# Kernel optimization log

Hardware: AMD Instinct MI355X
Metric: run time of the kernel (lower is better)

## Reference

```python
import math
import jax, jax.numpy as jnp
import numpy as np

B = 2
IN_DIM = 512
OUT_DIM = 256
MAX_IN_SEQ = 1024
MAX_OUT_SEQ = 512
SEQ = 1024  # actual_seq_len == max_in_seq
LN_EPS = 1e-5
TWO_PI = 2.0 * math.pi


def setup_inputs() -> dict:
    key = jax.random.key(0)
    ks = jax.random.split(key, 4)
    x = jax.random.normal(ks[0], (B * SEQ, IN_DIM), dtype=jnp.float32)
    M = jax.random.uniform(ks[1], (OUT_DIM, IN_DIM), minval=-0.5, maxval=0.5, dtype=jnp.float32)
    P = jax.random.uniform(ks[2], (OUT_DIM, OUT_DIM), minval=-0.1, maxval=0.1, dtype=jnp.float32)
    Linker = jax.random.uniform(ks[3], (MAX_IN_SEQ, MAX_OUT_SEQ), minval=-0.1, maxval=0.1, dtype=jnp.float32)
    ln_gamma = jnp.ones((OUT_DIM,), dtype=jnp.float32)
    ln_beta = jnp.zeros((OUT_DIM,), dtype=jnp.float32)
    return {"x": x, "M": M, "P": P, "Linker": Linker,
            "ln_gamma": ln_gamma, "ln_beta": ln_beta, "actual_seq_len": SEQ}


def _periods(out_dim):
    # periods[i, j] = i * out_dim + j + 2
    i = jnp.arange(out_dim, dtype=jnp.float32)[:, None]
    j = jnp.arange(out_dim, dtype=jnp.float32)[None, :]
    return i * out_dim + j + 2.0


def _layernorm(z, gamma, beta):
    mu = jnp.mean(z, axis=-1, keepdims=True)
    var = jnp.mean(jnp.square(z - mu), axis=-1, keepdims=True)
    return (z - mu) * jax.lax.rsqrt(var + LN_EPS) * gamma + beta


def reference(x, M, P, Linker, ln_gamma, ln_beta, actual_seq_len):
    total, _ = x.shape                      # (B*S, in_dim)
    batch = total // actual_seq_len
    out_seq = max(1, actual_seq_len // 2)   # reduction_factor = 2

    # projection + LayerNorm
    Z = x @ M.T                             # (B*S, out_dim)
    Zn = _layernorm(Z, ln_gamma, ln_beta)

    # position-dependent cos-weighted transform over the flattened B*S axis
    periods = _periods(OUT_DIM)             # (O, O)
    k = jnp.arange(total, dtype=jnp.float32)  # (B*S,)
    phi = jnp.cos(TWO_PI * k[:, None, None] / periods[None])  # (B*S, O, O)
    T = jnp.einsum('kj,ij,kij->ki', Zn, P, phi)               # (B*S, O)

    # adaptive sequence-length reduction via Linker
    AL = Linker[:actual_seq_len, :out_seq]  # (S, S')
    T3 = T.reshape(batch, actual_seq_len, OUT_DIM)
    U = jnp.einsum('bso,st->bto', T3, AL).reshape(batch * out_seq, OUT_DIM)

    # shared residual: reuse M and Linker on the pre-LN projection
    R3 = Z.reshape(batch, actual_seq_len, OUT_DIM)
    R = jnp.einsum('bso,st->bto', R3, AL).reshape(batch * out_seq, OUT_DIM)

    return U + R, out_seq
```

## Files before the change

### kernel.cpp

```cpp
#include <hip/hip_runtime.h>
#include <hip/hip_bf16.h>

#define TOT     2048
#define INDIM   512
#define OD      256
#define SEQL    1024
#define TQ      512
#define NB      2
#define LN_EPS  1e-5f

#define JSPL    16
#define JW      (OD / JSPL)
#define K3SPL   4

typedef __attribute__((ext_vector_type(8))) short bf16x8;
typedef __attribute__((ext_vector_type(4))) float f32x4;
typedef __attribute__((ext_vector_type(2))) float f32x2;

__device__ __forceinline__ short f2bf(float f) {
    __hip_bfloat16 h = __float2bfloat16(f);
    return *(short*)&h;
}
__device__ __forceinline__ uint pack2(float a, float b) {
    return (uint)(ushort)f2bf(a) | ((uint)(ushort)f2bf(b) << 16);
}

__global__ __launch_bounds__(256) void kALt(
    const float* __restrict__ L, short* __restrict__ ALt)
{
    __shared__ float tl[32][36];
    const int tt = blockIdx.x;
    const int s0 = (tt >> 4) * 32;
    const int t0 = (tt & 15) * 32;
    const int tid = threadIdx.x;
    const int r  = tid >> 3;
    const int c4 = (tid & 7) * 4;
    float4 v = *(const float4*)(L + (size_t)(s0 + r) * TQ + t0 + c4);
    tl[r][c4 + 0] = v.x; tl[r][c4 + 1] = v.y;
    tl[r][c4 + 2] = v.z; tl[r][c4 + 3] = v.w;
    __syncthreads();
    uint lo = pack2(tl[c4 + 0][r], tl[c4 + 1][r]);
    uint hi = pack2(tl[c4 + 2][r], tl[c4 + 3][r]);
    *(uint2*)(ALt + (size_t)(t0 + r) * SEQL + s0 + c4) = make_uint2(lo, hi);
}

template<bool CVT>
__device__ __forceinline__ void mfma_tile64(
    const void* __restrict__ Av, int lda,
    const void* __restrict__ Bv, int ldb,
    float* __restrict__ C, int ldc,
    int r0, int c0, int k0, int nk)
{
    __shared__ short Al[64][40];
    __shared__ short Bl[64][40];
    const int tid = threadIdx.x;
    const int w   = tid >> 6;
    const int wm  = w >> 1, wn = w & 1;
    const int l   = tid & 63;
    const int lr  = l & 15, lg = l >> 4;
    const int srow = tid >> 2, skg = (tid & 3) * 8;

    f32x4 acc[2][2] = {{{0.f,0.f,0.f,0.f},{0.f,0.f,0.f,0.f}},
                       {{0.f,0.f,0.f,0.f},{0.f,0.f,0.f,0.f}}};

    for (int ks = 0; ks < nk; ++ks) {
        const int kb = k0 + ks * 32;
        __syncthreads();
        if (CVT) {
            const float* Af = (const float*)Av;
            const float* Bf = (const float*)Bv;
            const float* ar = Af + (size_t)(r0 + srow) * lda + kb + skg;
            float4 a0 = *(const float4*)ar, a1 = *(const float4*)(ar + 4);
            *(uint4*)&Al[srow][skg] = make_uint4(pack2(a0.x, a0.y), pack2(a0.z, a0.w),
                                                 pack2(a1.x, a1.y), pack2(a1.z, a1.w));
            const float* br = Bf + (size_t)(c0 + srow) * ldb + kb + skg;
            float4 b0 = *(const float4*)br, b1 = *(const float4*)(br + 4);
            *(uint4*)&Bl[srow][skg] = make_uint4(pack2(b0.x, b0.y), pack2(b0.z, b0.w),
                                                 pack2(b1.x, b1.y), pack2(b1.z, b1.w));
        } else {
            const short* As = (const short*)Av;
            const short* Bs = (const short*)Bv;
            *(bf16x8*)&Al[srow][skg] = *(const bf16x8*)(As + (size_t)(r0 + srow) * lda + kb + skg);
            *(bf16x8*)&Bl[srow][skg] = *(const bf16x8*)(Bs + (size_t)(c0 + srow) * ldb + kb + skg);
        }
        __syncthreads();
        bf16x8 a0 = *(const bf16x8*)&Al[wm * 32 +      lr][lg * 8];
        bf16x8 a1 = *(const bf16x8*)&Al[wm * 32 + 16 + lr][lg * 8];
        bf16x8 b0 = *(const bf16x8*)&Bl[wn * 32 +      lr][lg * 8];
        bf16x8 b1 = *(const bf16x8*)&Bl[wn * 32 + 16 + lr][lg * 8];
        acc[0][0] = __builtin_amdgcn_mfma_f32_16x16x32_bf16(a0, b0, acc[0][0], 0, 0, 0);
        acc[0][1] = __builtin_amdgcn_mfma_f32_16x16x32_bf16(a0, b1, acc[0][1], 0, 0, 0);
        acc[1][0] = __builtin_amdgcn_mfma_f32_16x16x32_bf16(a1, b0, acc[1][0], 0, 0, 0);
        acc[1][1] = __builtin_amdgcn_mfma_f32_16x16x32_bf16(a1, b1, acc[1][1], 0, 0, 0);
    }
#pragma unroll
    for (int sm = 0; sm < 2; ++sm)
#pragma unroll
    for (int sn = 0; sn < 2; ++sn)
#pragma unroll
    for (int q = 0; q < 4; ++q)
        C[(size_t)(r0 + wm * 32 + sm * 16 + 4 * lg + q) * ldc
          + (c0 + wn * 32 + sn * 16 + lr)] = acc[sm][sn][q];
}

__global__ __launch_bounds__(256, 4) void k1_mfma(
    const float* __restrict__ x, const float* __restrict__ M,
    float* __restrict__ Zp)
{
    mfma_tile64<true>(x, INDIM, M, INDIM,
                      Zp + (size_t)blockIdx.z * TOT * OD, OD,
                      blockIdx.x * 64, blockIdx.y * 64, blockIdx.z * 256, 8);
}

__global__ __launch_bounds__(256) void k1b_ln(
    const float* __restrict__ Zp,
    const float* __restrict__ gamma, const float* __restrict__ beta,
    float* __restrict__ Z, float* __restrict__ Zn)
{
    const int r0 = blockIdx.x * 8;
    const int c  = threadIdx.x;

    float acc[8];
#pragma unroll
    for (int r = 0; r < 8; ++r) {
        const size_t i = (size_t)(r0 + r) * OD + c;
        acc[r] = Zp[i] + Zp[(size_t)TOT * OD + i];
    }

    __shared__ float s1[8][4], s2[8][4];
    const int lane = c & 63;
    const int wid  = c >> 6;
#pragma unroll
    for (int r = 0; r < 8; ++r) {
        float s = acc[r], q = acc[r] * acc[r];
#pragma unroll
        for (int off = 32; off > 0; off >>= 1) {
            s += __shfl_xor(s, off, 64);
            q += __shfl_xor(q, off, 64);
        }
        if (lane == 0) { s1[r][wid] = s; s2[r][wid] = q; }
    }
    __syncthreads();
#pragma unroll
    for (int r = 0; r < 8; ++r) {
        float s  = s1[r][0] + s1[r][1] + s1[r][2] + s1[r][3];
        float q  = s2[r][0] + s2[r][1] + s2[r][2] + s2[r][3];
        float mu = s * (1.f / OD);
        float var = q * (1.f / OD) - mu * mu;
        float inv = rsqrtf(var + LN_EPS);
        float z  = acc[r];
        float zn = (z - mu) * inv * gamma[c] + beta[c];
        Z [(size_t)(r0 + r) * OD + c] = z;
        Zn[(size_t)(r0 + r) * OD + c] = zn;
    }
}

__global__ __launch_bounds__(128) void k2_t(
    const float* __restrict__ Zn, const float* __restrict__ P,
    short* __restrict__ Tp)
{
    const int k0 = blockIdx.x * 64;
    const int i0 = blockIdx.y * 128;
    const int j0 = blockIdx.z * JW;

    __shared__ float znT[JW][68];
    __shared__ float ptT[JW][132];

    const int tid = threadIdx.x;
    {
        const int row = tid & 63;
        const int jh  = (tid >> 6) * 8;
        const float* zr = Zn + (size_t)(k0 + row) * OD + j0 + jh;
        float4 v0 = *(const float4*)(zr);
        float4 v1 = *(const float4*)(zr + 4);
        znT[jh + 0][row] = v0.x; znT[jh + 1][row] = v0.y;
        znT[jh + 2][row] = v0.z; znT[jh + 3][row] = v0.w;
        znT[jh + 4][row] = v1.x; znT[jh + 5][row] = v1.y;
        znT[jh + 6][row] = v1.z; znT[jh + 7][row] = v1.w;
        const float* pr = P + (size_t)(i0 + tid) * OD + j0;
        float4 p0 = *(const float4*)(pr);
        float4 p1 = *(const float4*)(pr + 4);
        float4 p2 = *(const float4*)(pr + 8);
        float4 p3 = *(const float4*)(pr + 12);
        ptT[ 0][tid] = p0.x; ptT[ 1][tid] = p0.y; ptT[ 2][tid] = p0.z; ptT[ 3][tid] = p0.w;
        ptT[ 4][tid] = p1.x; ptT[ 5][tid] = p1.y; ptT[ 6][tid] = p1.z; ptT[ 7][tid] = p1.w;
        ptT[ 8][tid] = p2.x; ptT[ 9][tid] = p2.y; ptT[10][tid] = p2.z; ptT[11][tid] = p2.w;
        ptT[12][tid] = p3.x; ptT[13][tid] = p3.y; ptT[14][tid] = p3.z; ptT[15][tid] = p3.w;
    }
    __syncthreads();

    const int kg = tid >> 6;
    const int l  = tid & 63;
    const int il = 2 * l;
    const float kbase = (float)(k0 + kg * 32);
    const float pbA   = (float)((i0 + il) * OD + j0 + 2);

    f32x2 accA[16], accB[16];
#pragma unroll
    for (int m = 0; m < 16; ++m) { accA[m] = (f32x2){0.f, 0.f}; accB[m] = (f32x2){0.f, 0.f}; }

    const float* zrow = &znT[0][kg * 32];

    for (int j = 0; j < JW; ++j) {
        f32x2 wp = *(const f32x2*)&ptT[j][il];
        const float pA  = pbA + (float)j;
        const float ipA = __builtin_amdgcn_rcpf(pA);
        const float aA  = __builtin_amdgcn_fractf(kbase * ipA);
        const float c0A = __builtin_amdgcn_cosf(aA);
        const float s0A = __builtin_amdgcn_sinf(aA);
        const float cdA = __builtin_amdgcn_cosf(ipA);
        const float sdA = __builtin_amdgcn_sinf(ipA);
        const float c1A = c0A * cdA - s0A * sdA;
        const float s1A = s0A * cdA + c0A * sdA;
        const float c2A = c1A * cdA - s1A * sdA;
        const float c3A = c2A * cdA - (s1A * cdA + c1A * sdA) * sdA;
        const float r2A = 2.f * (1.f - 2.f * sdA * sdA);
        f32x2 DA_p = {wp.x * c0A, wp.x * c1A};
        f32x2 DA_c = {wp.x * c2A, wp.x * c3A};
        const f32x2 RA = {r2A, r2A};
        const float pB  = pA + 256.f;
        const float ipB = __builtin_amdgcn_rcpf(pB);
        const float aB  = __builtin_amdgcn_fractf(kbase * ipB);
        const float c0B = __builtin_amdgcn_cosf(aB);
        const float s0B = __builtin_amdgcn_sinf(aB);
        const float cdB = __builtin_amdgcn_cosf(ipB);
        const float sdB = __builtin_amdgcn_sinf(ipB);
        const float c1B = c0B * cdB - s0B * sdB;
        const float s1B = s0B * cdB + c0B * sdB;
        const float c2B = c1B * cdB - s1B * sdB;
        const float c3B = c2B * cdB - (s1B * cdB + c1B * sdB) * sdB;
        const float r2B = 2.f * (1.f - 2.f * sdB * sdB);
        f32x2 DB_p = {wp.y * c0B, wp.y * c1B};
        f32x2 DB_c = {wp.y * c2B, wp.y * c3B};
        const f32x2 RB = {r2B, r2B};

        const float* zc = zrow + (size_t)j * 68;
#pragma unroll
        for (int m = 0; m < 8; ++m) {
            float4 z4 = *(const float4*)(zc + 4 * m);
            f32x2 zlo = {z4.x, z4.y};
            f32x2 zhi = {z4.z, z4.w};
            accA[2 * m    ] += zlo * DA_p;
            accB[2 * m    ] += zlo * DB_p;
            f32x2 tA = RA * DA_c - DA_p;  DA_p = DA_c;  DA_c = tA;
            f32x2 tB = RB * DB_c - DB_p;  DB_p = DB_c;  DB_c = tB;
            accA[2 * m + 1] += zhi * DA_p;
            accB[2 * m + 1] += zhi * DB_p;
            tA = RA * DA_c - DA_p;  DA_p = DA_c;  DA_c = tA;
            tB = RB * DB_c - DB_p;  DB_p = DB_c;  DB_c = tB;
        }
    }

    short* Tpl = Tp + (size_t)blockIdx.z * (TOT * OD);
    const int ia = i0 + il;
    const int kb = k0 + kg * 32;
#pragma unroll
    for (int m = 0; m < 16; ++m) {
        *(uint*)(Tpl + (size_t)(kb + 2 * m    ) * OD + ia) = pack2(accA[m].x, accB[m].x);
        *(uint*)(Tpl + (size_t)(kb + 2 * m + 1) * OD + ia) = pack2(accA[m].y, accB[m].y);
    }
}

__global__ __launch_bounds__(256) void k2b_w(
    const float* __restrict__ Z, const short* __restrict__ Tp,
    short* __restrict__ Wt)
{
    __shared__ float tl[32][36];
    const int kt0 = blockIdx.x * 32;
    const int o0  = blockIdx.y * 32;
    const int tid = threadIdx.x;
    const int r   = tid >> 3;
    const int c4  = (tid & 7) * 4;

    const size_t idx = (size_t)(kt0 + r) * OD + o0 + c4;
    float4 z = *(const float4*)(Z + idx);
#pragma unroll
    for (int p = 0; p < JSPL; ++p) {
        uint2 t = *(const uint2*)(Tp + (size_t)p * (TOT * OD) + idx);
        z.x += __uint_as_float(t.x << 16);
        z.y += __uint_as_float(t.x & 0xFFFF0000u);
        z.z += __uint_as_float(t.y << 16);
        z.w += __uint_as_float(t.y & 0xFFFF0000u);
    }
    *(float4*)&tl[r][c4] = z;
    __syncthreads();

    const int ol = tid >> 3;
    const int sc = (tid & 7) * 4;
    const int b  = kt0 >> 10;
    const int sb = kt0 & 1023;
    uint lo = pack2(tl[sc + 0][ol], tl[sc + 1][ol]);
    uint hi = pack2(tl[sc + 2][ol], tl[sc + 3][ol]);
    *(uint2*)(Wt + ((size_t)b * OD + o0 + ol) * SEQL + sb + sc) = make_uint2(lo, hi);
}

__global__ __launch_bounds__(256, 4) void k3_mfma(
    const short* __restrict__ ALt, const short* __restrict__ Wt,
    float* __restrict__ Op)
{
    const int b   = blockIdx.z & 1;
    const int ksp = blockIdx.z >> 1;
    mfma_tile64<false>(ALt, SEQL, Wt + (size_t)b * OD * SEQL, SEQL,
                       Op + (size_t)ksp * (NB * TQ * OD) + (size_t)b * TQ * OD, OD,
                       blockIdx.x * 64, blockIdx.y * 64, ksp * (SEQL / K3SPL), (SEQL / K3SPL) / 32);
}

__global__ __launch_bounds__(256) void k4_comb(
    const float* __restrict__ Op, float* __restrict__ out, int out_size)
{
    const int m = blockIdx.x * 256 + threadIdx.x;
    const int N4 = (NB * TQ * OD) / 4;
    if (m < N4) {
        float4 a = ((const float4*)Op)[m];
#pragma unroll
        for (int p = 1; p < K3SPL; ++p) {
            float4 t = ((const float4*)(Op + (size_t)p * (NB * TQ * OD)))[m];
            a.x += t.x; a.y += t.y; a.z += t.z; a.w += t.w;
        }
        ((float4*)out)[m] = a;
    }
    if (m == 0 && out_size > NB * TQ * OD)
        out[NB * TQ * OD] = (float)TQ;
}

extern "C" void kernel_launch(void* const* d_in, const int* in_sizes, int n_in,
                              void* d_out, int out_size, void* d_ws, size_t ws_size,
                              hipStream_t stream)
{
    const float* x  = (const float*)d_in[0];
    const float* M  = (const float*)d_in[1];
    const float* P  = (const float*)d_in[2];
    const float* L  = (const float*)d_in[3];
    const float* g  = (const float*)d_in[4];
    const float* be = (const float*)d_in[5];
    float* out = (float*)d_out;

    float* ws_f = (float*)d_ws;
    float* Zp = ws_f;
    float* Z  = Zp + 2 * (size_t)TOT * OD;
    float* Zn = Z  + (size_t)TOT * OD;
    float* Op = Zn + (size_t)TOT * OD;
    short* ALt = (short*)(Op + (size_t)K3SPL * NB * TQ * OD);
    short* Wt  = ALt + (size_t)TQ * SEQL;
    short* Tp  = Wt  + (size_t)NB * OD * SEQL;

    kALt<<<512, 256, 0, stream>>>(L, ALt);
    k1_mfma<<<dim3(TOT / 64, OD / 64, 2), 256, 0, stream>>>(x, M, Zp);
    k1b_ln<<<TOT / 8, 256, 0, stream>>>(Zp, g, be, Z, Zn);
    k2_t<<<dim3(TOT / 64, OD / 128, JSPL), 128, 0, stream>>>(Zn, P, Tp);
    k2b_w<<<dim3(TOT / 32, OD / 32), 256, 0, stream>>>(Z, Tp, Wt);
    k3_mfma<<<dim3(TQ / 64, OD / 64, NB * K3SPL), 256, 0, stream>>>(ALt, Wt, Op);
    k4_comb<<<(NB * TQ * OD / 4 + 255) / 256, 256, 0, stream>>>(Op, out, out_size);
}
```

Before: 48.95 us.

## Fuse LN, split-K reductions and Linker transpose into producer kernels via last-block counters

Collapses seven launches into a memset plus three kernels. The LN row statistics, the Tp partial sum, and the k3 split-K combine now run in whichever block finishes last for each tile, detected with an atomic counter and threadfence. LN normalization is applied on the fly when loading into k2, and k3 reads the fp32 Linker and W directly, transposing and converting them to bf16 in LDS. This removes launch overhead and intermediate buffers (Z, Zn, ALt, Wt), at the cost of tail work serialized in the last blocks and strided, uncoalesced LDS transposes in k3.

```diff
diff --git a/kernel.cpp b/kernel.cpp
--- a/kernel.cpp
+++ b/kernel.cpp
@@ -24,25 +24,8 @@
 __device__ __forceinline__ uint pack2(float a, float b) {
     return (uint)(ushort)f2bf(a) | ((uint)(ushort)f2bf(b) << 16);
 }
-
-__global__ __launch_bounds__(256) void kALt(
-    const float* __restrict__ L, short* __restrict__ ALt)
-{
-    __shared__ float tl[32][36];
-    const int tt = blockIdx.x;
-    const int s0 = (tt >> 4) * 32;
-    const int t0 = (tt & 15) * 32;
-    const int tid = threadIdx.x;
-    const int r  = tid >> 3;
-    const int c4 = (tid & 7) * 4;
-    float4 v = *(const float4*)(L + (size_t)(s0 + r) * TQ + t0 + c4);
-    tl[r][c4 + 0] = v.x; tl[r][c4 + 1] = v.y;
-    tl[r][c4 + 2] = v.z; tl[r][c4 + 3] = v.w;
-    __syncthreads();
-    uint lo = pack2(tl[c4 + 0][r], tl[c4 + 1][r]);
-    uint hi = pack2(tl[c4 + 2][r], tl[c4 + 3][r]);
-    *(uint2*)(ALt + (size_t)(t0 + r) * SEQL + s0 + c4) = make_uint2(lo, hi);
-}
+__device__ __forceinline__ float bflo(uint t) { return __uint_as_float(t << 16); }
+__device__ __forceinline__ float bfhi(uint t) { return __uint_as_float(t & 0xFFFF0000u); }
 
 template<bool CVT>
 __device__ __forceinline__ void mfma_tile64(
@@ -105,59 +88,46 @@
 
 __global__ __launch_bounds__(256, 4) void k1_mfma(
     const float* __restrict__ x, const float* __restrict__ M,
-    float* __restrict__ Zp)
+    float* __restrict__ Zp, float* __restrict__ muv, float* __restrict__ inv,
+    int* __restrict__ cnt)
 {
     mfma_tile64<true>(x, INDIM, M, INDIM,
                       Zp + (size_t)blockIdx.z * TOT * OD, OD,
                       blockIdx.x * 64, blockIdx.y * 64, blockIdx.z * 256, 8);
-}
-
-__global__ __launch_bounds__(256) void k1b_ln(
-    const float* __restrict__ Zp,
+
+    __threadfence();
+    __syncthreads();
+    __shared__ int lastf;
+    if (threadIdx.x == 0)
+        lastf = (atomicAdd(&cnt[blockIdx.x], 1) == 7);
+    __syncthreads();
+    if (!lastf) return;
+
+    const int row  = blockIdx.x * 64 + (threadIdx.x >> 2);
+    const int part = threadIdx.x & 3;
+    const float* z0 = Zp + (size_t)row * OD + part * 64;
+    const float* z1 = z0 + (size_t)TOT * OD;
+    float s = 0.f, q = 0.f;
+#pragma unroll 8
+    for (int c = 0; c < 64; ++c) {
+        float v = z0[c] + z1[c];
+        s += v; q += v * v;
+    }
+    s += __shfl_xor(s, 1); q += __shfl_xor(q, 1);
+    s += __shfl_xor(s, 2); q += __shfl_xor(q, 2);
+    if (part == 0) {
+        float m  = s * (1.f / OD);
+        float vr = q * (1.f / OD) - m * m;
+        muv[row] = m;
+        inv[row] = rsqrtf(vr + LN_EPS);
+    }
+}
+
+__global__ __launch_bounds__(128) void k2_t(
+    const float* __restrict__ Zp, const float* __restrict__ muv, const float* __restrict__ inv,
     const float* __restrict__ gamma, const float* __restrict__ beta,
-    float* __restrict__ Z, float* __restrict__ Zn)
-{
-    const int r0 = blockIdx.x * 8;
-    const int c  = threadIdx.x;
-
-    float acc[8];
-#pragma unroll
-    for (int r = 0; r < 8; ++r) {
-        const size_t i = (size_t)(r0 + r) * OD + c;
-        acc[r] = Zp[i] + Zp[(size_t)TOT * OD + i];
-    }
-
-    __shared__ float s1[8][4], s2[8][4];
-    const int lane = c & 63;
-    const int wid  = c >> 6;
-#pragma unroll
-    for (int r = 0; r < 8; ++r) {
-        float s = acc[r], q = acc[r] * acc[r];
-#pragma unroll
-        for (int off = 32; off > 0; off >>= 1) {
-            s += __shfl_xor(s, off, 64);
-            q += __shfl_xor(q, off, 64);
-        }
-        if (lane == 0) { s1[r][wid] = s; s2[r][wid] = q; }
-    }
-    __syncthreads();
-#pragma unroll
-    for (int r = 0; r < 8; ++r) {
-        float s  = s1[r][0] + s1[r][1] + s1[r][2] + s1[r][3];
-        float q  = s2[r][0] + s2[r][1] + s2[r][2] + s2[r][3];
-        float mu = s * (1.f / OD);
-        float var = q * (1.f / OD) - mu * mu;
-        float inv = rsqrtf(var + LN_EPS);
-        float z  = acc[r];
-        float zn = (z - mu) * inv * gamma[c] + beta[c];
-        Z [(size_t)(r0 + r) * OD + c] = z;
-        Zn[(size_t)(r0 + r) * OD + c] = zn;
-    }
-}
-
-__global__ __launch_bounds__(128) void k2_t(
-    const float* __restrict__ Zn, const float* __restrict__ P,
-    short* __restrict__ Tp)
+    const float* __restrict__ P, short* __restrict__ Tp,
+    float* __restrict__ W, int* __restrict__ cnt)
 {
     const int k0 = blockIdx.x * 64;
     const int i0 = blockIdx.y * 128;
@@ -170,13 +140,25 @@
     {
         const int row = tid & 63;
         const int jh  = (tid >> 6) * 8;
-        const float* zr = Zn + (size_t)(k0 + row) * OD + j0 + jh;
-        float4 v0 = *(const float4*)(zr);
-        float4 v1 = *(const float4*)(zr + 4);
-        znT[jh + 0][row] = v0.x; znT[jh + 1][row] = v0.y;
-        znT[jh + 2][row] = v0.z; znT[jh + 3][row] = v0.w;
-        znT[jh + 4][row] = v1.x; znT[jh + 5][row] = v1.y;
-        znT[jh + 6][row] = v1.z; znT[jh + 7][row] = v1.w;
+        const size_t base = (size_t)(k0 + row) * OD + j0 + jh;
+        float4 a0 = *(const float4*)(Zp + base);
+        float4 a1 = *(const float4*)(Zp + base + 4);
+        float4 b0 = *(const float4*)(Zp + (size_t)TOT * OD + base);
+        float4 b1 = *(const float4*)(Zp + (size_t)TOT * OD + base + 4);
+        const float m  = muv[k0 + row];
+        const float iv = inv[k0 + row];
+        float4 g0 = *(const float4*)(gamma + j0 + jh);
+        float4 g1 = *(const float4*)(gamma + j0 + jh + 4);
+        float4 e0 = *(const float4*)(beta + j0 + jh);
+        float4 e1 = *(const float4*)(beta + j0 + jh + 4);
+        znT[jh + 0][row] = (a0.x + b0.x - m) * iv * g0.x + e0.x;
+        znT[jh + 1][row] = (a0.y + b0.y - m) * iv * g0.y + e0.y;
+        znT[jh + 2][row] = (a0.z + b0.z - m) * iv * g0.z + e0.z;
+        znT[jh + 3][row] = (a0.w + b0.w - m) * iv * g0.w + e0.w;
+        znT[jh + 4][row] = (a1.x + b1.x - m) * iv * g1.x + e1.x;
+        znT[jh + 5][row] = (a1.y + b1.y - m) * iv * g1.y + e1.y;
+        znT[jh + 6][row] = (a1.z + b1.z - m) * iv * g1.z + e1.z;
+        znT[jh + 7][row] = (a1.w + b1.w - m) * iv * g1.w + e1.w;
         const float* pr = P + (size_t)(i0 + tid) * OD + j0;
         float4 p0 = *(const float4*)(pr);
         float4 p1 = *(const float4*)(pr + 4);
@@ -259,67 +241,120 @@
         *(uint*)(Tpl + (size_t)(kb + 2 * m    ) * OD + ia) = pack2(accA[m].x, accB[m].x);
         *(uint*)(Tpl + (size_t)(kb + 2 * m + 1) * OD + ia) = pack2(accA[m].y, accB[m].y);
     }
-}
-
-__global__ __launch_bounds__(256) void k2b_w(
-    const float* __restrict__ Z, const short* __restrict__ Tp,
-    short* __restrict__ Wt)
-{
-    __shared__ float tl[32][36];
-    const int kt0 = blockIdx.x * 32;
-    const int o0  = blockIdx.y * 32;
-    const int tid = threadIdx.x;
-    const int r   = tid >> 3;
-    const int c4  = (tid & 7) * 4;
-
-    const size_t idx = (size_t)(kt0 + r) * OD + o0 + c4;
-    float4 z = *(const float4*)(Z + idx);
-#pragma unroll
-    for (int p = 0; p < JSPL; ++p) {
-        uint2 t = *(const uint2*)(Tp + (size_t)p * (TOT * OD) + idx);
-        z.x += __uint_as_float(t.x << 16);
-        z.y += __uint_as_float(t.x & 0xFFFF0000u);
-        z.z += __uint_as_float(t.y << 16);
-        z.w += __uint_as_float(t.y & 0xFFFF0000u);
-    }
-    *(float4*)&tl[r][c4] = z;
-    __syncthreads();
-
-    const int ol = tid >> 3;
-    const int sc = (tid & 7) * 4;
-    const int b  = kt0 >> 10;
-    const int sb = kt0 & 1023;
-    uint lo = pack2(tl[sc + 0][ol], tl[sc + 1][ol]);
-    uint hi = pack2(tl[sc + 2][ol], tl[sc + 3][ol]);
-    *(uint2*)(Wt + ((size_t)b * OD + o0 + ol) * SEQL + sb + sc) = make_uint2(lo, hi);
+
+    __threadfence();
+    __syncthreads();
+    __shared__ int lastf;
+    if (tid == 0)
+        lastf = (atomicAdd(&cnt[blockIdx.x * 2 + blockIdx.y], 1) == JSPL - 1);
+    __syncthreads();
+    if (!lastf) return;
+
+#pragma unroll
+    for (int e = 0; e < 32; ++e) {
+        const int lin = e * 128 + tid;
+        const int r   = lin >> 6;
+        const int c2  = (lin & 63) * 2;
+        const size_t addr = (size_t)(k0 + r) * OD + i0 + c2;
+        float wx = Zp[addr]     + Zp[(size_t)TOT * OD + addr];
+        float wy = Zp[addr + 1] + Zp[(size_t)TOT * OD + addr + 1];
+#pragma unroll
+        for (int p = 0; p < JSPL; ++p) {
+            uint t = *(const uint*)(Tp + (size_t)p * (TOT * OD) + addr);
+            wx += bflo(t); wy += bfhi(t);
+        }
+        *(f32x2*)(W + addr) = (f32x2){wx, wy};
+    }
 }
 
 __global__ __launch_bounds__(256, 4) void k3_mfma(
-    const short* __restrict__ ALt, const short* __restrict__ Wt,
-    float* __restrict__ Op)
+    const float* __restrict__ L, const float* __restrict__ W,
+    float* __restrict__ Op, float* __restrict__ out, int out_size,
+    int* __restrict__ cnt)
 {
     const int b   = blockIdx.z & 1;
     const int ksp = blockIdx.z >> 1;
-    mfma_tile64<false>(ALt, SEQL, Wt + (size_t)b * OD * SEQL, SEQL,
-                       Op + (size_t)ksp * (NB * TQ * OD) + (size_t)b * TQ * OD, OD,
-                       blockIdx.x * 64, blockIdx.y * 64, ksp * (SEQL / K3SPL), (SEQL / K3SPL) / 32);
-}
-
-__global__ __launch_bounds__(256) void k4_comb(
-    const float* __restrict__ Op, float* __restrict__ out, int out_size)
-{
-    const int m = blockIdx.x * 256 + threadIdx.x;
-    const int N4 = (NB * TQ * OD) / 4;
-    if (m < N4) {
-        float4 a = ((const float4*)Op)[m];
+    const int r0  = blockIdx.x * 64;
+    const int c0  = blockIdx.y * 64;
+    const int k0  = ksp * (SEQL / K3SPL);
+
+    __shared__ short Al[64][40];
+    __shared__ short Bl[64][40];
+    const int tid = threadIdx.x;
+    const int w   = tid >> 6;
+    const int wm  = w >> 1, wn = w & 1;
+    const int l   = tid & 63;
+    const int lr  = l & 15, lg = l >> 4;
+    const int sq  = tid >> 3;
+    const int tc  = (tid & 7) * 8;
+
+    f32x4 acc[2][2] = {{{0.f,0.f,0.f,0.f},{0.f,0.f,0.f,0.f}},
+                       {{0.f,0.f,0.f,0.f},{0.f,0.f,0.f,0.f}}};
+
+    const float* Wb = W + (size_t)b * SEQL * OD;
+
+    for (int ks = 0; ks < (SEQL / K3SPL) / 32; ++ks) {
+        const int kb = k0 + ks * 32;
+        __syncthreads();
+        {
+            const float* ar = L + (size_t)(kb + sq) * TQ + r0 + tc;
+            float4 a0 = *(const float4*)ar, a1 = *(const float4*)(ar + 4);
+            Al[tc + 0][sq] = f2bf(a0.x); Al[tc + 1][sq] = f2bf(a0.y);
+            Al[tc + 2][sq] = f2bf(a0.z); Al[tc + 3][sq] = f2bf(a0.w);
+            Al[tc + 4][sq] = f2bf(a1.x); Al[tc + 5][sq] = f2bf(a1.y);
+            Al[tc + 6][sq] = f2bf(a1.z); Al[tc + 7][sq] = f2bf(a1.w);
+            const float* br = Wb + (size_t)(kb + sq) * OD + c0 + tc;
+            float4 b0 = *(const float4*)br, b1 = *(const float4*)(br + 4);
+            Bl[tc + 0][sq] = f2bf(b0.x); Bl[tc + 1][sq] = f2bf(b0.y);
+            Bl[tc + 2][sq] = f2bf(b0.z); Bl[tc + 3][sq] = f2bf(b0.w);
+            Bl[tc + 4][sq] = f2bf(b1.x); Bl[tc + 5][sq] = f2bf(b1.y);
+            Bl[tc + 6][sq] = f2bf(b1.z); Bl[tc + 7][sq] = f2bf(b1.w);
+        }
+        __syncthreads();
+        bf16x8 a0 = *(const bf16x8*)&Al[wm * 32 +      lr][lg * 8];
+        bf16x8 a1 = *(const bf16x8*)&Al[wm * 32 + 16 + lr][lg * 8];
+        bf16x8 b0 = *(const bf16x8*)&Bl[wn * 32 +      lr][lg * 8];
+        bf16x8 b1 = *(const bf16x8*)&Bl[wn * 32 + 16 + lr][lg * 8];
+        acc[0][0] = __builtin_amdgcn_mfma_f32_16x16x32_bf16(a0, b0, acc[0][0], 0, 0, 0);
+        acc[0][1] = __builtin_amdgcn_mfma_f32_16x16x32_bf16(a0, b1, acc[0][1], 0, 0, 0);
+        acc[1][0] = __builtin_amdgcn_mfma_f32_16x16x32_bf16(a1, b0, acc[1][0], 0, 0, 0);
+        acc[1][1] = __builtin_amdgcn_mfma_f32_16x16x32_bf16(a1, b1, acc[1][1], 0, 0, 0);
+    }
+
+    float* Cp = Op + (size_t)ksp * (NB * TQ * OD) + (size_t)b * TQ * OD;
+#pragma unroll
+    for (int sm = 0; sm < 2; ++sm)
+#pragma unroll
+    for (int sn = 0; sn < 2; ++sn)
+#pragma unroll
+    for (int q = 0; q < 4; ++q)
+        Cp[(size_t)(r0 + wm * 32 + sm * 16 + 4 * lg + q) * OD
+           + (c0 + wn * 32 + sn * 16 + lr)] = acc[sm][sn][q];
+
+    __threadfence();
+    __syncthreads();
+    __shared__ int lastf;
+    if (tid == 0)
+        lastf = (atomicAdd(&cnt[(blockIdx.x * 4 + blockIdx.y) * 2 + b], 1) == K3SPL - 1);
+    __syncthreads();
+    if (!lastf) return;
+
+#pragma unroll
+    for (int e = 0; e < 4; ++e) {
+        const int lin = e * 256 + tid;
+        const int r   = lin >> 4;
+        const int c4  = (lin & 15) * 4;
+        const size_t addr = ((size_t)(b * TQ) + r0 + r) * OD + c0 + c4;
+        float4 a = *(const float4*)(Op + addr);
 #pragma unroll
         for (int p = 1; p < K3SPL; ++p) {
-            float4 t = ((const float4*)(Op + (size_t)p * (NB * TQ * OD)))[m];
+            float4 t = *(const float4*)(Op + (size_t)p * (NB * TQ * OD) + addr);
             a.x += t.x; a.y += t.y; a.z += t.z; a.w += t.w;
         }
-        ((float4*)out)[m] = a;
-    }
-    if (m == 0 && out_size > NB * TQ * OD)
+        *(float4*)(out + addr) = a;
+    }
+    if (tid == 0 && blockIdx.x == 0 && blockIdx.y == 0 && b == 0
+        && out_size > NB * TQ * OD)
         out[NB * TQ * OD] = (float)TQ;
 }
 
@@ -335,20 +370,20 @@
     const float* be = (const float*)d_in[5];
     float* out = (float*)d_out;
 
-    float* ws_f = (float*)d_ws;
-    float* Zp = ws_f;
-    float* Z  = Zp + 2 * (size_t)TOT * OD;
-    float* Zn = Z  + (size_t)TOT * OD;
-    float* Op = Zn + (size_t)TOT * OD;
-    short* ALt = (short*)(Op + (size_t)K3SPL * NB * TQ * OD);
-    short* Wt  = ALt + (size_t)TQ * SEQL;
-    short* Tp  = Wt  + (size_t)NB * OD * SEQL;
-
-    kALt<<<512, 256, 0, stream>>>(L, ALt);
-    k1_mfma<<<dim3(TOT / 64, OD / 64, 2), 256, 0, stream>>>(x, M, Zp);
-    k1b_ln<<<TOT / 8, 256, 0, stream>>>(Zp, g, be, Z, Zn);
-    k2_t<<<dim3(TOT / 64, OD / 128, JSPL), 128, 0, stream>>>(Zn, P, Tp);
-    k2b_w<<<dim3(TOT / 32, OD / 32), 256, 0, stream>>>(Z, Tp, Wt);
-    k3_mfma<<<dim3(TQ / 64, OD / 64, NB * K3SPL), 256, 0, stream>>>(ALt, Wt, Op);
-    k4_comb<<<(NB * TQ * OD / 4 + 255) / 256, 256, 0, stream>>>(Op, out, out_size);
-}
+    int*   cnt  = (int*)d_ws;
+    int*   cnt1 = cnt;
+    int*   cnt2 = cnt + 32;
+    int*   cnt3 = cnt + 96;
+    float* base = (float*)d_ws + 256;
+    float* Zp  = base;
+    float* W   = Zp + 2 * (size_t)TOT * OD;
+    float* Op  = W  + (size_t)TOT * OD;
+    float* muv = Op + (size_t)K3SPL * NB * TQ * OD;
+    float* inv = muv + TOT;
+    short* Tp  = (short*)(inv + TOT);
+
+    hipMemsetAsync(cnt, 0, 160 * sizeof(int), stream);
+    k1_mfma<<<dim3(TOT / 64, OD / 64, 2), 256, 0, stream>>>(x, M, Zp, muv, inv, cnt1);
+    k2_t<<<dim3(TOT / 64, OD / 128, JSPL), 128, 0, stream>>>(Zp, muv, inv, g, be, P, Tp, W, cnt2);
+    k3_mfma<<<dim3(TQ / 64, OD / 64, NB * K3SPL), 256, 0, stream>>>(L, W, Op, out, out_size, cnt3);
+}
```

Result: slower. 168.8 us (+244.9%).
